# Kernel optimization log

Measured on AMD Instinct MI355X. Metric: run time of the kernel, lower is better.

The kernel has to match this reference:

```python
import jax, jax.numpy as jnp
import numpy as np

FEATURE_DIM = 4
LOSS_WEIGHT = 1.0
DELTA_V = 0.5
DELTA_D = 1.5
NUM_INST = 16  # labels 0..15 all present w.h.p. -> torch.unique yields exactly these


def _safe_norm(x, axis):
    # L2 norm with zero-safe gradient (relu clamp downstream kills grad anyway)
    sq = jnp.sum(x * x, axis=axis)
    return jnp.where(sq > 0, jnp.sqrt(jnp.where(sq > 0, sq, 1.0)), 0.0)


def _forward_single(emb, instance, kernel, training_mask):
    # emb: [D, H, W]; instance/kernel/training_mask: [H, W]
    D, K = FEATURE_DIM, NUM_INST
    tm = (training_mask > 0.5).astype(jnp.int32)
    kn = (kernel > 0.5).astype(jnp.int32)
    inst = instance * tm                      # [H, W]
    inst_k = (inst * kn).reshape(-1)          # [N]
    inst = inst.reshape(-1)                   # [N]
    embf = emb.reshape(D, -1).T               # [N, D]

    # per-instance mean over kernel pixels (scatter-mean); label 0 stays zero
    cnt_k = jax.ops.segment_sum(jnp.ones(inst_k.shape, jnp.float32), inst_k, K)
    sum_k = jax.ops.segment_sum(embf, inst_k, K)          # [K, D]
    emb_mean = sum_k / jnp.maximum(cnt_k, 1.0)[:, None]
    emb_mean = emb_mean.at[0].set(0.0)

    # l_agg: per-pixel distance to own-instance mean, segment-mean per label
    dist = _safe_norm(embf - emb_mean[inst], axis=1)       # [N]
    val = jnp.log(jax.nn.relu(dist - DELTA_V) ** 2 + 1.0)
    cnt = jax.ops.segment_sum(jnp.ones(inst.shape, jnp.float32), inst, K)
    agg = jax.ops.segment_sum(val, inst, K) / jnp.maximum(cnt, 1.0)
    l_agg = jnp.mean(agg[1:])

    # l_dis: pairwise means, excluding diagonal and label 0
    diff = emb_mean[:, None, :] - emb_mean[None, :, :]     # [K, K, D]
    pd = _safe_norm(diff, axis=-1)
    pv = jnp.log(jax.nn.relu(2.0 * DELTA_D - pd) ** 2 + 1.0)
    mask = 1.0 - jnp.eye(K, dtype=jnp.float32)
    mask = mask.at[0, :].set(0.0).at[:, 0].set(0.0)
    l_dis = jnp.sum(pv * mask) / ((K - 1) * (K - 2))

    # l_reg: mean log(||mean_i|| + 1) over ALL K columns (incl. zero col 0)
    l_reg = jnp.mean(jnp.log(_safe_norm(emb_mean, axis=1) + 1.0)) * 0.001

    return l_agg + l_dis + l_reg


def reference(emb, instance, kernel, training_mask, bboxes):
    # bboxes is accepted but unused, as in the original forward
    loss_batch = jax.vmap(_forward_single)(emb, instance, kernel, training_mask)
    return jnp.mean(LOSS_WEIGHT * loss_batch)


def setup_inputs() -> dict:
    key = jax.random.key(0)
    k1, k2, k3, k4, k5 = jax.random.split(key, 5)
    B, H, W = 8, 640, 640
    return {
        "emb": jax.random.normal(k1, (B, FEATURE_DIM, H, W), jnp.float32),
        "instance": jax.random.randint(k2, (B, H, W), 0, NUM_INST, jnp.int32),
        "kernel": jax.random.uniform(k3, (B, H, W), dtype=jnp.float32),
        "training_mask": jax.random.uniform(k4, (B, H, W), dtype=jnp.float32),
        "bboxes": jax.random.uniform(k5, (B, 201, 4), dtype=jnp.float32),
    }
```

## Files before the change

### kernel.cpp

```cpp
#include <hip/hip_runtime.h>
#include <math.h>

#define NUM_K 16
#define DELTA_V 0.5f
#define DELTA_D 1.5f


#define BPB 200
#define QSTRIDE (BPB * 256)


__global__ __launch_bounds__(256) void pass1_kernel(
    const float* __restrict__ emb, const int* __restrict__ inst,
    const float* __restrict__ kern, const float* __restrict__ tmask,
    float* __restrict__ cntk, float* __restrict__ sumk, int N)
{
    __shared__ float s_h[75 * 17];
    for (int i = threadIdx.x; i < 75 * 17; i += 256) s_h[i] = 0.f;
    __syncthreads();

    const int tid  = threadIdx.x;
    const int b    = blockIdx.x / BPB;
    const int wb   = blockIdx.x % BPB;
    const int copy = tid & 15;

    const size_t base = (size_t)b * N;
    const int4*   iv4 = (const int4*)(inst + base);
    const float4* kv4 = (const float4*)(kern + base);
    const float4* tv4 = (const float4*)(tmask + base);
    const float4* e0v = (const float4*)(emb + ((size_t)b * 4 + 0) * N);
    const float4* e1v = (const float4*)(emb + ((size_t)b * 4 + 1) * N);
    const float4* e2v = (const float4*)(emb + ((size_t)b * 4 + 2) * N);
    const float4* e3v = (const float4*)(emb + ((size_t)b * 4 + 3) * N);

    const int g0 = wb * 256 + tid;
    const int g1 = g0 + QSTRIDE;

    const int4   ivA = iv4[g0], ivB = iv4[g1];
    const float4 kvA = kv4[g0], kvB = kv4[g1];
    const float4 tvA = tv4[g0], tvB = tv4[g1];
    const float4 a0A = e0v[g0], a0B = e0v[g1];
    const float4 a1A = e1v[g0], a1B = e1v[g1];
    const float4 a2A = e2v[g0], a2B = e2v[g1];
    const float4 a3A = e3v[g0], a3B = e3v[g1];

    #define ACC1(iv, kv, tv, a0, a1, a2, a3, px)                               \
        {                                                                      \
            const int lab = iv.px;                                             \
            if (lab > 0 && tv.px > 0.5f && kv.px > 0.5f) {                     \
                float* p = &s_h[(lab - 1) * 85 + copy];           \
                atomicAdd(p +  0, a0.px);                                      \
                atomicAdd(p + 17, a1.px);                                      \
                atomicAdd(p + 34, a2.px);                                      \
                atomicAdd(p + 51, a3.px);                                      \
                atomicAdd(p + 68, 1.f);                                        \
            }                                                                  \
        }
    ACC1(ivA, kvA, tvA, a0A, a1A, a2A, a3A, x)
    ACC1(ivA, kvA, tvA, a0A, a1A, a2A, a3A, y)
    ACC1(ivA, kvA, tvA, a0A, a1A, a2A, a3A, z)
    ACC1(ivA, kvA, tvA, a0A, a1A, a2A, a3A, w)
    ACC1(ivB, kvB, tvB, a0B, a1B, a2B, a3B, x)
    ACC1(ivB, kvB, tvB, a0B, a1B, a2B, a3B, y)
    ACC1(ivB, kvB, tvB, a0B, a1B, a2B, a3B, z)
    ACC1(ivB, kvB, tvB, a0B, a1B, a2B, a3B, w)
    #undef ACC1

    __syncthreads();

    if (tid < 75) {
        float s = 0.f;
        #pragma unroll
        for (int c = 0; c < 16; ++c) s += s_h[tid * 17 + c];
        if (s != 0.f) {
            const int k = tid / 5 + 1, v = tid % 5;
            if (v < 4) atomicAdd(&sumk[(b * NUM_K + k) * 4 + v], s);
            else       atomicAdd(&cntk[b * NUM_K + k], s);
        }
    }
}

__global__ __launch_bounds__(256) void pass2_kernel(
    const float* __restrict__ emb, const int* __restrict__ inst,
    const float* __restrict__ tmask,
    const float* __restrict__ cntk, const float* __restrict__ sumk,
    float* __restrict__ vsum, float* __restrict__ vcnt, int N)
{
    __shared__ float  s_h[30 * 17];
    __shared__ float4 s_mean[NUM_K];

    for (int i = threadIdx.x; i < 30 * 17; i += 256) s_h[i] = 0.f;

    const int tid = threadIdx.x;
    const int b   = blockIdx.x / BPB;
    const int wb  = blockIdx.x % BPB;

    if (tid < 64) {
        const int k = tid >> 2, d = tid & 3;
        const float c = cntk[b * NUM_K + k];
        const float m = (k == 0) ? 0.f
                                 : sumk[(b * NUM_K + k) * 4 + d] / fmaxf(c, 1.f);
        ((float*)&s_mean[k])[d] = m;
    }
    __syncthreads();

    const int copy = tid & 15;

    const size_t base = (size_t)b * N;
    const int4*   iv4 = (const int4*)(inst + base);
    const float4* tv4 = (const float4*)(tmask + base);
    const float4* e0v = (const float4*)(emb + ((size_t)b * 4 + 0) * N);
    const float4* e1v = (const float4*)(emb + ((size_t)b * 4 + 1) * N);
    const float4* e2v = (const float4*)(emb + ((size_t)b * 4 + 2) * N);
    const float4* e3v = (const float4*)(emb + ((size_t)b * 4 + 3) * N);

    const int g0 = wb * 256 + tid;
    const int g1 = g0 + QSTRIDE;

    const int4   ivA = iv4[g0], ivB = iv4[g1];
    const float4 tvA = tv4[g0], tvB = tv4[g1];
    const float4 a0A = e0v[g0], a0B = e0v[g1];
    const float4 a1A = e1v[g0], a1B = e1v[g1];
    const float4 a2A = e2v[g0], a2B = e2v[g1];
    const float4 a3A = e3v[g0], a3B = e3v[g1];

    #define ACC2(iv, tv, a0, a1, a2, a3, px)                                   \
        {                                                                      \
            const int lab = (tv.px > 0.5f) ? iv.px : 0;                        \
            if (lab > 0) {                                                     \
                const float4 mu = s_mean[lab];                                 \
                const float dx = a0.px - mu.x;                                 \
                const float dy = a1.px - mu.y;                                 \
                const float dz = a2.px - mu.z;                                 \
                const float dw = a3.px - mu.w;                                 \
                const float dist = sqrtf(dx*dx + dy*dy + dz*dz + dw*dw);       \
                const float r   = fmaxf(dist - DELTA_V, 0.f);                  \
                const float val = logf(fmaf(r, r, 1.f));                       \
                float* p = &s_h[(lab - 1) * 34 + copy];           \
                atomicAdd(p,      val);                                        \
                atomicAdd(p + 17, 1.f);                                        \
            }                                                                  \
        }
    ACC2(ivA, tvA, a0A, a1A, a2A, a3A, x)
    ACC2(ivA, tvA, a0A, a1A, a2A, a3A, y)
    ACC2(ivA, tvA, a0A, a1A, a2A, a3A, z)
    ACC2(ivA, tvA, a0A, a1A, a2A, a3A, w)
    ACC2(ivB, tvB, a0B, a1B, a2B, a3B, x)
    ACC2(ivB, tvB, a0B, a1B, a2B, a3B, y)
    ACC2(ivB, tvB, a0B, a1B, a2B, a3B, z)
    ACC2(ivB, tvB, a0B, a1B, a2B, a3B, w)
    #undef ACC2

    __syncthreads();

    if (tid < 30) {
        float s = 0.f;
        #pragma unroll
        for (int c = 0; c < 16; ++c) s += s_h[tid * 17 + c];
        if (s != 0.f) {
            const int k = (tid >> 1) + 1;
            if ((tid & 1) == 0) atomicAdd(&vsum[b * NUM_K + k], s);
            else                atomicAdd(&vcnt[b * NUM_K + k], s);
        }
    }
}

__global__ __launch_bounds__(128) void finalize_kernel(
    const float* __restrict__ cntk, const float* __restrict__ sumk,
    const float* __restrict__ vsum, const float* __restrict__ vcnt,
    float* __restrict__ out, int B)
{
    __shared__ float s_mean[8][NUM_K][4];
    __shared__ float s_part[128];

    const int t = threadIdx.x;
    const int b = t >> 4;
    const int k = t & 15;

    const float c = cntk[t];
    float m0 = 0.f, m1 = 0.f, m2 = 0.f, m3 = 0.f;
    if (k != 0) {
        const float inv = 1.f / fmaxf(c, 1.f);
        m0 = sumk[t * 4 + 0] * inv;
        m1 = sumk[t * 4 + 1] * inv;
        m2 = sumk[t * 4 + 2] * inv;
        m3 = sumk[t * 4 + 3] * inv;
    }
    s_mean[b][k][0] = m0; s_mean[b][k][1] = m1;
    s_mean[b][k][2] = m2; s_mean[b][k][3] = m3;
    __syncthreads();

    float partial = 0.f;

    if (k >= 1) {
        const float agg = vsum[t] / fmaxf(vcnt[t], 1.f);
        partial += agg / 15.f;
    }

    if (k >= 1) {
        #pragma unroll
        for (int j = 1; j < NUM_K; ++j) {
            if (j == k) continue;
            const float dx = m0 - s_mean[b][j][0];
            const float dy = m1 - s_mean[b][j][1];
            const float dz = m2 - s_mean[b][j][2];
            const float dw = m3 - s_mean[b][j][3];
            const float pd = sqrtf(dx*dx + dy*dy + dz*dz + dw*dw);
            const float r  = fmaxf(2.f * DELTA_D - pd, 0.f);
            partial += logf(r * r + 1.f) / 210.f;
        }
    }

    {
        const float nrm = sqrtf(m0*m0 + m1*m1 + m2*m2 + m3*m3);
        partial += logf(nrm + 1.f) * (0.001f / 16.f);
    }

    s_part[t] = partial;
    __syncthreads();

    if (t == 0) {
        float s = 0.f;
        for (int i = 0; i < 128; ++i) s += s_part[i];
        out[0] = s / (float)B;
    }
}

extern "C" void kernel_launch(void* const* d_in, const int* in_sizes, int n_in,
                              void* d_out, int out_size, void* d_ws, size_t ws_size,
                              hipStream_t stream) {
    const float* emb   = (const float*)d_in[0];
    const int*   inst  = (const int*)d_in[1];
    const float* kern  = (const float*)d_in[2];
    const float* tmask = (const float*)d_in[3];

    const int B = 8;
    const int N = in_sizes[1] / B;

    float* ws   = (float*)d_ws;
    float* cntk = ws;
    float* sumk = ws + 128;
    float* vsum = ws + 640;
    float* vcnt = ws + 768;
    float* outf = (float*)d_out;

    hipMemsetAsync(d_ws, 0, 896 * sizeof(float), stream);

    pass1_kernel<<<dim3(BPB * 8), dim3(256), 0, stream>>>(
        emb, inst, kern, tmask, cntk, sumk, N);
    pass2_kernel<<<dim3(BPB * 8), dim3(256), 0, stream>>>(
        emb, inst, tmask, cntk, sumk, vsum, vcnt, N);
    finalize_kernel<<<dim3(1), dim3(128), 0, stream>>>(
        cntk, sumk, vsum, vcnt, outf, B);
}
```

Before: 157.8 us.

## Replace global atomics with per-block partials and a deterministic reduce kernel

Each block now writes its per-label partial sums to a staging array in the workspace instead of issuing global atomicAdds. A new small kernel reduces the pass-1 partials and computes the per-instance means once, and the finalize kernel reduces the pass-2 partials. This removes the memset and the global atomic contention, and pass2 no longer recomputes the means. The cost is one extra kernel launch and extra reads of the staging buffers in serial single-block or 8-block reductions.

```diff
diff --git a/kernel.cpp b/kernel.cpp
--- a/kernel.cpp
+++ b/kernel.cpp
@@ -5,15 +5,17 @@
 #define DELTA_V 0.5f
 #define DELTA_D 1.5f
 
-
 #define BPB 200
 #define QSTRIDE (BPB * 256)
 
+#define S1OFF 0
+#define S2OFF 128000
+#define MVOFF 179200
 
 __global__ __launch_bounds__(256) void pass1_kernel(
     const float* __restrict__ emb, const int* __restrict__ inst,
     const float* __restrict__ kern, const float* __restrict__ tmask,
-    float* __restrict__ cntk, float* __restrict__ sumk, int N)
+    float* __restrict__ stage1, int N)
 {
     __shared__ float s_h[75 * 17];
     for (int i = threadIdx.x; i < 75 * 17; i += 256) s_h[i] = 0.f;
@@ -48,7 +50,7 @@
         {                                                                      \
             const int lab = iv.px;                                             \
             if (lab > 0 && tv.px > 0.5f && kv.px > 0.5f) {                     \
-                float* p = &s_h[(lab - 1) * 85 + copy];           \
+                float* p = &s_h[(lab - 1) * 85 + copy];                        \
                 atomicAdd(p +  0, a0.px);                                      \
                 atomicAdd(p + 17, a1.px);                                      \
                 atomicAdd(p + 34, a2.px);                                      \
@@ -68,23 +70,49 @@
 
     __syncthreads();
 
-    if (tid < 75) {
-        float s = 0.f;
+    if (tid < 80) {
+        float s = 0.f;
+        if (tid < 75) {
+            #pragma unroll
+            for (int c = 0; c < 16; ++c) s += s_h[tid * 17 + c];
+        }
+        stage1[b * 16000 + tid * 200 + wb] = s;
+    }
+}
+
+__global__ __launch_bounds__(256) void reduce_means_kernel(
+    const float* __restrict__ stage1, float* __restrict__ meanv)
+{
+    __shared__ float rs[80];
+    const int b = blockIdx.x, tid = threadIdx.x;
+    const int w = tid >> 6, lane = tid & 63;
+
+    for (int r = w; r < 80; r += 4) {
+        const float* p = stage1 + b * 16000 + r * 200;
+        float s = 0.f;
+        for (int j = lane; j < 200; j += 64) s += p[j];
         #pragma unroll
-        for (int c = 0; c < 16; ++c) s += s_h[tid * 17 + c];
-        if (s != 0.f) {
-            const int k = tid / 5 + 1, v = tid % 5;
-            if (v < 4) atomicAdd(&sumk[(b * NUM_K + k) * 4 + v], s);
-            else       atomicAdd(&cntk[b * NUM_K + k], s);
-        }
+        for (int m = 32; m > 0; m >>= 1) s += __shfl_xor(s, m, 64);
+        if (lane == 0) rs[r] = s;
+    }
+    __syncthreads();
+
+    if (tid < 64) {
+        const int k = tid >> 2, d = tid & 3;
+        float mv = 0.f;
+        if (k > 0) {
+            const float s = rs[(k - 1) * 5 + d];
+            const float c = rs[(k - 1) * 5 + 4];
+            mv = s / fmaxf(c, 1.f);
+        }
+        meanv[b * 64 + tid] = mv;
     }
 }
 
 __global__ __launch_bounds__(256) void pass2_kernel(
     const float* __restrict__ emb, const int* __restrict__ inst,
-    const float* __restrict__ tmask,
-    const float* __restrict__ cntk, const float* __restrict__ sumk,
-    float* __restrict__ vsum, float* __restrict__ vcnt, int N)
+    const float* __restrict__ tmask, const float* __restrict__ meanv,
+    float* __restrict__ stage2, int N)
 {
     __shared__ float  s_h[30 * 17];
     __shared__ float4 s_mean[NUM_K];
@@ -95,13 +123,7 @@
     const int b   = blockIdx.x / BPB;
     const int wb  = blockIdx.x % BPB;
 
-    if (tid < 64) {
-        const int k = tid >> 2, d = tid & 3;
-        const float c = cntk[b * NUM_K + k];
-        const float m = (k == 0) ? 0.f
-                                 : sumk[(b * NUM_K + k) * 4 + d] / fmaxf(c, 1.f);
-        ((float*)&s_mean[k])[d] = m;
-    }
+    if (tid < 64) ((float*)&s_mean[0])[tid] = meanv[b * 64 + tid];
     __syncthreads();
 
     const int copy = tid & 15;
@@ -136,7 +158,7 @@
                 const float dist = sqrtf(dx*dx + dy*dy + dz*dz + dw*dw);       \
                 const float r   = fmaxf(dist - DELTA_V, 0.f);                  \
                 const float val = logf(fmaf(r, r, 1.f));                       \
-                float* p = &s_h[(lab - 1) * 34 + copy];           \
+                float* p = &s_h[(lab - 1) * 34 + copy];                        \
                 atomicAdd(p,      val);                                        \
                 atomicAdd(p + 17, 1.f);                                        \
             }                                                                  \
@@ -153,76 +175,76 @@
 
     __syncthreads();
 
-    if (tid < 30) {
-        float s = 0.f;
+    if (tid < 32) {
+        float s = 0.f;
+        if (tid < 30) {
+            #pragma unroll
+            for (int c = 0; c < 16; ++c) s += s_h[tid * 17 + c];
+        }
+        stage2[b * 6400 + tid * 200 + wb] = s;
+    }
+}
+
+__global__ __launch_bounds__(256) void finalize_kernel(
+    const float* __restrict__ stage2, const float* __restrict__ meanv,
+    float* __restrict__ out)
+{
+    __shared__ float rs2[240];
+    __shared__ float sm[512];
+    __shared__ float s_part[128];
+
+    const int tid = threadIdx.x;
+    const int w = tid >> 6, lane = tid & 63;
+
+    for (int r = w; r < 240; r += 4) {
+        const int bb = r / 30, rr = r % 30;
+        const float* p = stage2 + bb * 6400 + rr * 200;
+        float s = 0.f;
+        for (int j = lane; j < 200; j += 64) s += p[j];
         #pragma unroll
-        for (int c = 0; c < 16; ++c) s += s_h[tid * 17 + c];
-        if (s != 0.f) {
-            const int k = (tid >> 1) + 1;
-            if ((tid & 1) == 0) atomicAdd(&vsum[b * NUM_K + k], s);
-            else                atomicAdd(&vcnt[b * NUM_K + k], s);
-        }
-    }
-}
-
-__global__ __launch_bounds__(128) void finalize_kernel(
-    const float* __restrict__ cntk, const float* __restrict__ sumk,
-    const float* __restrict__ vsum, const float* __restrict__ vcnt,
-    float* __restrict__ out, int B)
-{
-    __shared__ float s_mean[8][NUM_K][4];
-    __shared__ float s_part[128];
-
-    const int t = threadIdx.x;
-    const int b = t >> 4;
-    const int k = t & 15;
-
-    const float c = cntk[t];
-    float m0 = 0.f, m1 = 0.f, m2 = 0.f, m3 = 0.f;
-    if (k != 0) {
-        const float inv = 1.f / fmaxf(c, 1.f);
-        m0 = sumk[t * 4 + 0] * inv;
-        m1 = sumk[t * 4 + 1] * inv;
-        m2 = sumk[t * 4 + 2] * inv;
-        m3 = sumk[t * 4 + 3] * inv;
-    }
-    s_mean[b][k][0] = m0; s_mean[b][k][1] = m1;
-    s_mean[b][k][2] = m2; s_mean[b][k][3] = m3;
-    __syncthreads();
-
-    float partial = 0.f;
-
-    if (k >= 1) {
-        const float agg = vsum[t] / fmaxf(vcnt[t], 1.f);
-        partial += agg / 15.f;
-    }
-
-    if (k >= 1) {
-        #pragma unroll
-        for (int j = 1; j < NUM_K; ++j) {
-            if (j == k) continue;
-            const float dx = m0 - s_mean[b][j][0];
-            const float dy = m1 - s_mean[b][j][1];
-            const float dz = m2 - s_mean[b][j][2];
-            const float dw = m3 - s_mean[b][j][3];
-            const float pd = sqrtf(dx*dx + dy*dy + dz*dz + dw*dw);
-            const float r  = fmaxf(2.f * DELTA_D - pd, 0.f);
-            partial += logf(r * r + 1.f) / 210.f;
-        }
-    }
-
-    {
-        const float nrm = sqrtf(m0*m0 + m1*m1 + m2*m2 + m3*m3);
-        partial += logf(nrm + 1.f) * (0.001f / 16.f);
-    }
-
-    s_part[t] = partial;
-    __syncthreads();
-
-    if (t == 0) {
+        for (int m = 32; m > 0; m >>= 1) s += __shfl_xor(s, m, 64);
+        if (lane == 0) rs2[r] = s;
+    }
+    sm[tid]       = meanv[tid];
+    sm[tid + 256] = meanv[tid + 256];
+    __syncthreads();
+
+    if (tid < 128) {
+        const int bb = tid >> 4, k = tid & 15;
+        const float m0 = sm[tid * 4 + 0], m1 = sm[tid * 4 + 1];
+        const float m2 = sm[tid * 4 + 2], m3 = sm[tid * 4 + 3];
+        float partial = 0.f;
+
+        if (k >= 1) {
+            const float vs = rs2[bb * 30 + (k - 1) * 2 + 0];
+            const float vc = rs2[bb * 30 + (k - 1) * 2 + 1];
+            partial += (vs / fmaxf(vc, 1.f)) / 15.f;
+        }
+        if (k >= 1) {
+            #pragma unroll
+            for (int j = 1; j < NUM_K; ++j) {
+                if (j == k) continue;
+                const float dx = m0 - sm[(bb * 16 + j) * 4 + 0];
+                const float dy = m1 - sm[(bb * 16 + j) * 4 + 1];
+                const float dz = m2 - sm[(bb * 16 + j) * 4 + 2];
+                const float dw = m3 - sm[(bb * 16 + j) * 4 + 3];
+                const float pd = sqrtf(dx*dx + dy*dy + dz*dz + dw*dw);
+                const float r  = fmaxf(2.f * DELTA_D - pd, 0.f);
+                partial += logf(r * r + 1.f) / 210.f;
+            }
+        }
+        {
+            const float nrm = sqrtf(m0*m0 + m1*m1 + m2*m2 + m3*m3);
+            partial += logf(nrm + 1.f) * (0.001f / 16.f);
+        }
+        s_part[tid] = partial;
+    }
+    __syncthreads();
+
+    if (tid == 0) {
         float s = 0.f;
         for (int i = 0; i < 128; ++i) s += s_part[i];
-        out[0] = s / (float)B;
+        out[0] = s / 8.f;
     }
 }
 
@@ -234,22 +256,18 @@
     const float* kern  = (const float*)d_in[2];
     const float* tmask = (const float*)d_in[3];
 
-    const int B = 8;
-    const int N = in_sizes[1] / B;
-
-    float* ws   = (float*)d_ws;
-    float* cntk = ws;
-    float* sumk = ws + 128;
-    float* vsum = ws + 640;
-    float* vcnt = ws + 768;
-    float* outf = (float*)d_out;
-
-    hipMemsetAsync(d_ws, 0, 896 * sizeof(float), stream);
+    const int N = in_sizes[1] / 8;
+
+    float* ws     = (float*)d_ws;
+    float* stage1 = ws + S1OFF;
+    float* stage2 = ws + S2OFF;
+    float* meanv  = ws + MVOFF;
+    float* outf   = (float*)d_out;
 
     pass1_kernel<<<dim3(BPB * 8), dim3(256), 0, stream>>>(
-        emb, inst, kern, tmask, cntk, sumk, N);
+        emb, inst, kern, tmask, stage1, N);
+    reduce_means_kernel<<<dim3(8), dim3(256), 0, stream>>>(stage1, meanv);
     pass2_kernel<<<dim3(BPB * 8), dim3(256), 0, stream>>>(
-        emb, inst, tmask, cntk, sumk, vsum, vcnt, N);
-    finalize_kernel<<<dim3(1), dim3(128), 0, stream>>>(
-        cntk, sumk, vsum, vcnt, outf, B);
-}
+        emb, inst, tmask, meanv, stage2, N);
+    finalize_kernel<<<dim3(1), dim3(256), 0, stream>>>(stage2, meanv, outf);
+}
```

Measured after the change: 237.2 us. 1.5x slower.
